# Kernel tuning notes

Hardware: AMD Instinct MI355X
Metric: run time of the kernel (lower is better)

Reference implementation:

```python
import jax, jax.numpy as jnp
import numpy as np

B, S, V, E, H = 256, 512, 800, 128, 256

def setup_inputs() -> dict:
    key = jax.random.key(0)
    ks = jax.random.split(key, 16)
    def rn(k, shape, scale=0.05):
        return jax.random.normal(k, shape, dtype=jnp.float32) * scale
    return {
        "x": jax.random.randint(ks[0], (B, S), 0, V),
        "emb": rn(ks[1], (V, E), 1.0),
        "Wih0": rn(ks[2], (4 * H, E)),
        "Whh0": rn(ks[3], (4 * H, H)),
        "bih0": rn(ks[4], (4 * H,)),
        "bhh0": rn(ks[5], (4 * H,)),
        "Wih1": rn(ks[6], (4 * H, H)),
        "Whh1": rn(ks[7], (4 * H, H)),
        "bih1": rn(ks[8], (4 * H,)),
        "bhh1": rn(ks[9], (4 * H,)),
        "ln_g": jnp.ones((H,), jnp.float32),
        "ln_b": jnp.zeros((H,), jnp.float32),
        "proj_W": rn(ks[10], (E, H)),
        "proj_b": rn(ks[11], (E,)),
    }

def _lstm_layer(x, Wih, Whh, bih, bhh):
    # x: [B, S, D]; returns full hidden sequence [B, S, H]
    b, s, _ = x.shape
    h0 = jnp.zeros((b, H), x.dtype)
    c0 = jnp.zeros((b, H), x.dtype)
    # precompute input projections for all timesteps: [S, B, 4H]
    xp = jnp.einsum("bsd,gd->sbg", x, Wih) + bih + bhh

    def step(carry, xp_t):
        h, c = carry
        gates = xp_t + h @ Whh.T  # [B, 4H]
        i, f, g, o = jnp.split(gates, 4, axis=-1)  # torch gate order i,f,g,o
        i = jax.nn.sigmoid(i)
        f = jax.nn.sigmoid(f)
        g = jnp.tanh(g)
        o = jax.nn.sigmoid(o)
        c = f * c + i * g
        h = o * jnp.tanh(c)
        return (h, c), h

    (_, _), hs = jax.lax.scan(step, (h0, c0), xp)
    return hs.transpose(1, 0, 2)  # [B, S, H]

def reference(x, emb, Wih0, Whh0, bih0, bhh0, Wih1, Whh1, bih1, bhh1, ln_g, ln_b, proj_W, proj_b):
    table = emb.at[0].set(0.0)  # padding_idx=0
    e = table[x]  # [B, S, E]
    h1 = _lstm_layer(e, Wih0, Whh0, bih0, bhh0)
    h2 = _lstm_layer(h1, Wih1, Whh1, bih1, bhh1)
    hn = h2[:, -1, :]  # h_n[-1]: last layer, final timestep [B, H]
    mu = jnp.mean(hn, axis=-1, keepdims=True)
    var = jnp.mean(jnp.square(hn - mu), axis=-1, keepdims=True)
    y = (hn - mu) * jax.lax.rsqrt(var + 1e-5) * ln_g + ln_b
    return y @ proj_W.T + proj_b  # [B, 128]
```

## Files before the change

### kernel.cpp

```cpp
#include <hip/hip_runtime.h>
#include <hip/hip_bf16.h>


typedef unsigned short u16;
typedef unsigned int   u32;
using short8 = __attribute__((ext_vector_type(8))) short;
using f32x4  = __attribute__((ext_vector_type(4))) float;

#define NB 256
#define NS 512
#define NE 128
#define NH 256
#define NG 1024

#define WLDS_FRAGS 18
#define HOFF 147456
#define SCAN_LDS (HOFF + 2 * 16 * NH * 2)

#define L2E     1.4426950408889634f
#define TWO_L2E 2.8853900817779268f

__device__ __forceinline__ u16 f2b(float x) {
  __hip_bfloat16 h = __float2bfloat16(x);
  return __builtin_bit_cast(u16, h);
}
__device__ __forceinline__ float b2f(u16 u) {
  return __builtin_bit_cast(float, (u32)u << 16);
}
__device__ __forceinline__ float ex2(float x)  { return __builtin_amdgcn_exp2f(x); }
__device__ __forceinline__ float ex2n(float x) { return __builtin_amdgcn_exp2f(-x); }
__device__ __forceinline__ float rcpa(float x) { return __builtin_amdgcn_rcpf(x); }

__global__ __launch_bounds__(256) void prep_weights(
    const float* Wih0, const float* Whh0, const float* bih0, const float* bhh0,
    const float* Wih1, const float* Whh1, const float* bih1, const float* bhh1,
    u16* wih0b, u16* whh0b, u16* wih1b, u16* whh1b, float* bc0, float* bc1) {
  int stride = gridDim.x * blockDim.x;
  int tid = blockIdx.x * blockDim.x + threadIdx.x;
  for (int i = tid; i < NG * NE; i += stride) {
    float s = (((i >> 7) >> 8) == 2) ? TWO_L2E : L2E;
    wih0b[i] = f2b(Wih0[i] * s);
  }
  for (int i = tid; i < NG * NH; i += stride) {
    float s = (((i >> 8) >> 8) == 2) ? TWO_L2E : L2E;
    whh0b[i] = f2b(Whh0[i] * s);
    wih1b[i] = f2b(Wih1[i] * s);
    whh1b[i] = f2b(Whh1[i] * s);
  }
  for (int i = tid; i < NG; i += stride) {
    float s = ((i >> 8) == 2) ? TWO_L2E : L2E;
    bc0[i] = (bih0[i] + bhh0[i]) * s;
    bc1[i] = (bih1[i] + bhh1[i]) * s;
  }
}

__global__ __launch_bounds__(256) void embed_chunk(const int* __restrict__ x,
                                                   const float* __restrict__ emb,
                                                   u16* __restrict__ ebuf, int t0) {
  int gid = blockIdx.x * 256 + threadIdx.x;
  int d4 = gid & 31;
  int sb = gid >> 5;
  int b  = sb & (NB - 1);
  int sl = sb >> 8;
  int tok = x[b * NS + (t0 + sl)];
  float4 v = make_float4(0.f, 0.f, 0.f, 0.f);
  if (tok != 0) v = *(const float4*)(emb + (size_t)tok * NE + d4 * 4);
  ushort4 o;
  o.x = f2b(v.x); o.y = f2b(v.y); o.z = f2b(v.z); o.w = f2b(v.w);
  *(ushort4*)(ebuf + (size_t)sb * NE + d4 * 4) = o;
}

template <int K>
__global__ __launch_bounds__(256) void xp_gemm(const u16* __restrict__ A,
                                               const u16* __restrict__ W,
                                               const float* __restrict__ bias,
                                               u16* __restrict__ Cout) {
  __shared__ __align__(16) char lds[2 * 128 * 80];
  char* Asm = lds;
  char* Bsm = lds + 128 * 80;
  int tid = threadIdx.x;
  int w = tid >> 6, l = tid & 63;
  int hi = l >> 4, lo = l & 15;
  int mblk = blockIdx.x >> 3, nblk = blockIdx.x & 7;
  size_t arow0 = (size_t)mblk * 128;
  int g0 = nblk * 128;
  int wm = (w >> 1) * 64, wn = (w & 1) * 64;
  f32x4 acc[4][4] = {};
  int r = tid >> 1, cp = tid & 1;

  for (int k0 = 0; k0 < K; k0 += 32) {
    int4 a0 = *(const int4*)(A + (arow0 + r) * K + k0 + cp * 16);
    int4 a1 = *(const int4*)(A + (arow0 + r) * K + k0 + cp * 16 + 8);
    int4 b0 = *(const int4*)(W + (size_t)(g0 + r) * K + k0 + cp * 16);
    int4 b1 = *(const int4*)(W + (size_t)(g0 + r) * K + k0 + cp * 16 + 8);
    *(int4*)(Asm + r * 80 + cp * 32)      = a0;
    *(int4*)(Asm + r * 80 + cp * 32 + 16) = a1;
    *(int4*)(Bsm + r * 80 + cp * 32)      = b0;
    *(int4*)(Bsm + r * 80 + cp * 32 + 16) = b1;
    __syncthreads();
    short8 af[4], bfr[4];
#pragma unroll
    for (int mt = 0; mt < 4; ++mt)
      af[mt] = *(const short8*)(Asm + (wm + mt * 16 + lo) * 80 + hi * 16);
#pragma unroll
    for (int nt = 0; nt < 4; ++nt)
      bfr[nt] = *(const short8*)(Bsm + (wn + nt * 16 + lo) * 80 + hi * 16);
#pragma unroll
    for (int mt = 0; mt < 4; ++mt)
#pragma unroll
      for (int nt = 0; nt < 4; ++nt)
        acc[mt][nt] = __builtin_amdgcn_mfma_f32_16x16x32_bf16(af[mt], bfr[nt], acc[mt][nt], 0, 0, 0);
    __syncthreads();
  }
#pragma unroll
  for (int nt = 0; nt < 4; ++nt) {
    int gc = g0 + wn + nt * 16 + lo;
    float bv = bias[gc];
    int ws_ = (gc >> 4) & 7, mts = gc >> 7, his = (gc >> 2) & 3, rs = gc & 3;
    size_t gbase = ((size_t)(ws_ * 8 + mts) << 8) + (size_t)(his * 16) * 4 + rs;
#pragma unroll
    for (int mt = 0; mt < 4; ++mt) {
      size_t row = arow0 + wm + mt * 16 + hi * 4;
#pragma unroll
      for (int rr = 0; rr < 4; ++rr) {
        size_t rw = row + rr;
        int t = (int)(rw >> 8), ba = (int)(rw & 255);
        size_t e = ((size_t)(t * 16 + (ba >> 4)) << 14) + gbase + (size_t)(ba & 15) * 4;
        Cout[e] = f2b(acc[mt][nt][rr] + bv);
      }
    }
  }
}

__global__ __launch_bounds__(512, 2)
void scan_stage(const u16* __restrict__ xpA, const u16* __restrict__ whhA,
                u16* __restrict__ houtA, float* __restrict__ hsA,
                float* __restrict__ csA, int firstA, int activeA,
                const u16* __restrict__ xpB, const u16* __restrict__ whhB,
                float* __restrict__ hsB, float* __restrict__ csB,
                int firstB, int activeB,
                const int* __restrict__ x, const float* __restrict__ emb,
                const u16* __restrict__ wih0b, const float* __restrict__ bc0,
                u16* __restrict__ xpC, int t0c, int activeC, int T) {
  extern __shared__ __align__(16) char smem[];
  int bid = blockIdx.x;
  int tid = threadIdx.x;

  if (bid >= 32) {
    if (!activeC) return;
    int team = tid >> 8, tt = tid & 255;
    char* Asm = smem + team * 40960;
    char* Bsm = Asm + 20480;
    int wq = tt >> 6, lq = tt & 63;
    int hiq = lq >> 4, loq = lq & 15;
    int wm = (wq >> 1) * 64, wn = (wq & 1) * 64;
    int r = tt >> 1, cp = tt & 1;
    int njobs = T * 16;
    for (int j = (bid - 32) * 2 + team; j < njobs; j += 64) {
      int mblk = j >> 3, nblk = j & 7;
      size_t arow0 = (size_t)mblk * 128;
      int g0 = nblk * 128;
      f32x4 acc[4][4] = {};
      int rw = (int)(arow0 + r);
      int sl = rw >> 8, ba = rw & 255;
      int tok = x[ba * NS + t0c + sl];
      const float* erow = emb + (size_t)tok * NE;
      for (int k0 = 0; k0 < NE; k0 += 32) {
        const float* src = erow + k0 + cp * 16;
        u32 pk[8];
#pragma unroll
        for (int q = 0; q < 8; ++q) {
          float a = src[2 * q], b = src[2 * q + 1];
          if (tok == 0) { a = 0.0f; b = 0.0f; }
          pk[q] = (u32)f2b(a) | ((u32)f2b(b) << 16);
        }
        *(int4*)(Asm + r * 80 + cp * 32)      = *(int4*)&pk[0];
        *(int4*)(Asm + r * 80 + cp * 32 + 16) = *(int4*)&pk[4];
        int4 b0 = *(const int4*)(wih0b + (size_t)(g0 + r) * NE + k0 + cp * 16);
        int4 b1 = *(const int4*)(wih0b + (size_t)(g0 + r) * NE + k0 + cp * 16 + 8);
        *(int4*)(Bsm + r * 80 + cp * 32)      = b0;
        *(int4*)(Bsm + r * 80 + cp * 32 + 16) = b1;
        __syncthreads();
        short8 af[4], bfr[4];
#pragma unroll
        for (int mt = 0; mt < 4; ++mt)
          af[mt] = *(const short8*)(Asm + (wm + mt * 16 + loq) * 80 + hiq * 16);
#pragma unroll
        for (int nt = 0; nt < 4; ++nt)
          bfr[nt] = *(const short8*)(Bsm + (wn + nt * 16 + loq) * 80 + hiq * 16);
#pragma unroll
        for (int mt = 0; mt < 4; ++mt)
#pragma unroll
          for (int nt = 0; nt < 4; ++nt)
            acc[mt][nt] = __builtin_amdgcn_mfma_f32_16x16x32_bf16(af[mt], bfr[nt], acc[mt][nt], 0, 0, 0);
        __syncthreads();
      }
#pragma unroll
      for (int nt = 0; nt < 4; ++nt) {
        int gc = g0 + wn + nt * 16 + loq;
        float bv = bc0[gc];
        int ws_ = (gc >> 4) & 7, mts = gc >> 7, his = (gc >> 2) & 3, rs = gc & 3;
        size_t gbase = ((size_t)(ws_ * 8 + mts) << 8) + (size_t)(his * 16) * 4 + rs;
#pragma unroll
        for (int mt = 0; mt < 4; ++mt) {
          size_t row = arow0 + wm + mt * 16 + hiq * 4;
#pragma unroll
          for (int rr = 0; rr < 4; ++rr) {
            size_t rw2 = row + rr;
            int t = (int)(rw2 >> 8), ba2 = (int)(rw2 & 255);
            size_t e = ((size_t)(t * 16 + (ba2 >> 4)) << 14) + gbase + (size_t)(ba2 & 15) * 4;
            xpC[e] = f2b(acc[mt][nt][rr] + bv);
          }
        }
      }
    }
    return;
  }

  int roleB = bid >> 4;
  if (roleB ? !activeB : !activeA) return;
  const u16* xp      = roleB ? xpB  : xpA;
  const u16* whh     = roleB ? whhB : whhA;
  u16*       hout    = roleB ? (u16*)0 : houtA;
  float*     h_state = roleB ? hsB : hsA;
  float*     c_state = roleB ? csB : csA;
  int        first   = roleB ? firstB : firstA;
  int bgi = bid & 15;
  int bg = bgi * 16;

  int w = tid >> 6, l = tid & 63;
  int hi = l >> 4, lo = l & 15;

  int wbase = w * (WLDS_FRAGS * 1024) + l * 16;
  short8 wfv[8][5];
  short8 wfv2[6];
#pragma unroll
  for (int mt = 0; mt < 8; ++mt) {
#pragma unroll
    for (int p = 0; p < 8; ++p) {
      const u16* src = whh + (size_t)(16 * (w + 8 * mt) + lo) * NH + p * 32 + hi * 8;
      short8 v = *(const short8*)src;
      if (p < 2)                 *(short8*)(smem + wbase + (p * 8 + mt) * 1024) = v;
      else if (p == 2 && mt < 2) *(short8*)(smem + wbase + (16 + mt) * 1024) = v;
      else if (p == 2)           wfv2[mt - 2] = v;
      else                       wfv[mt][p - 3] = v;
    }
  }

  float c[2][4];
  if (first) {
    for (int i = tid; i < 16 * NH / 2; i += 512) ((u32*)(smem + HOFF))[i] = 0;
#pragma unroll
    for (int g = 0; g < 2; ++g)
#pragma unroll
      for (int r = 0; r < 4; ++r) c[g][r] = 0.0f;
  } else {
    for (int i = tid; i < 16 * NH; i += 512) {
      int b = i >> 8, k = i & 255;
      int p = k >> 5, hp = (k >> 3) & 3, kp = k & 7;
      int xx = hp * 16 + b;
      u16 hb = f2b(h_state[(size_t)(bg + b) * NH + k]);
      *(u16*)(smem + HOFF + p * 1024 + (xx ^ ((xx >> 3) & 7)) * 16 + kp * 2) = hb;
    }
#pragma unroll
    for (int g = 0; g < 2; ++g)
#pragma unroll
      for (int r = 0; r < 4; ++r) {
        int j = 16 * w + 128 * g + hi * 4 + r;
        c[g][r] = c_state[(size_t)(bg + lo) * NH + j];
      }
  }
  __syncthreads();

  int rdoff = (l ^ ((l >> 3) & 7)) * 16;
  int wroff[2];
#pragma unroll
  for (int g = 0; g < 2; ++g) {
    int xx = (2 * (w & 1) + (hi >> 1)) * 16 + lo;
    wroff[g] = (4 * g + (w >> 1)) * 1024 + (xx ^ ((xx >> 3) & 7)) * 16 + 8 * (hi & 1);
  }
  int bq = tid >> 5, kc = tid & 31;
  int xw = (kc & 3) * 16 + bq;
  int wboff = (kc >> 2) * 1024 + (xw ^ ((xw >> 3) & 7)) * 16;
  size_t wb_glob = (size_t)(bg + bq) * NH + kc * 8;

  const u16* xpp = xp + ((size_t)(bgi * 8 + w) * 2048) + (size_t)l * 4;

  ushort4 xq[8];
#pragma unroll
  for (int mt = 0; mt < 8; ++mt) xq[mt] = *(const ushort4*)(xpp + mt * 256);

  f32x4 acc[8];
  for (int t = 0; t < T; ++t) {
    int rbase = HOFF + ((t & 1) << 13);
    int wbbase = HOFF + ((~t & 1) << 13);
#pragma unroll
    for (int mt = 0; mt < 8; ++mt) {
      f32x4 a;
      a[0] = b2f(xq[mt].x); a[1] = b2f(xq[mt].y);
      a[2] = b2f(xq[mt].z); a[3] = b2f(xq[mt].w);
      acc[mt] = a;
    }
    xpp += 262144;
#pragma unroll
    for (int mt = 0; mt < 8; ++mt) xq[mt] = *(const ushort4*)(xpp + mt * 256);
#pragma unroll
    for (int p = 0; p < 8; ++p) {
      short8 bf = *(const short8*)(smem + rbase + rdoff + p * 1024);
#pragma unroll
      for (int mt = 0; mt < 8; ++mt) {
        short8 af;
        if (p < 2)                 af = *(const short8*)(smem + wbase + (p * 8 + mt) * 1024);
        else if (p == 2 && mt < 2) af = *(const short8*)(smem + wbase + (16 + mt) * 1024);
        else if (p == 2)           af = wfv2[mt - 2];
        else                       af = wfv[mt][p - 3];
        acc[mt] = __builtin_amdgcn_mfma_f32_16x16x32_bf16(af, bf, acc[mt], 0, 0, 0);
      }
    }
#pragma unroll
    for (int g = 0; g < 2; ++g) {
      float hv[4];
#pragma unroll
      for (int r = 0; r < 4; ++r) {
        float iv = rcpa(1.0f + ex2n(acc[g][r]));
        float fv = rcpa(1.0f + ex2n(acc[2 + g][r]));
        float gv = 1.0f - 2.0f * rcpa(ex2(acc[4 + g][r]) + 1.0f);
        float ov = rcpa(1.0f + ex2n(acc[6 + g][r]));
        float cc = fv * c[g][r] + iv * gv;
        c[g][r] = cc;
        float th = 1.0f - 2.0f * rcpa(ex2(cc * TWO_L2E) + 1.0f);
        hv[r] = ov * th;
      }
      u32 d0, d1;
      asm("v_cvt_pk_bf16_f32 %0, %1, %2" : "=v"(d0) : "v"(hv[0]), "v"(hv[1]));
      asm("v_cvt_pk_bf16_f32 %0, %1, %2" : "=v"(d1) : "v"(hv[2]), "v"(hv[3]));
      uint2 hw; hw.x = d0; hw.y = d1;
      *(uint2*)(smem + wbbase + wroff[g]) = hw;
    }
    __syncthreads();
    if (hout) {
      int4 hv4 = *(const int4*)(smem + wbbase + wboff);
      *(int4*)(hout + wb_glob + ((size_t)t << 16)) = hv4;
    }
  }

  int fbuf = HOFF + ((T & 1) << 13);
#pragma unroll
  for (int g = 0; g < 2; ++g) {
    ushort4 hv4 = *(const ushort4*)(smem + fbuf + wroff[g]);
    int j = 16 * w + 128 * g + 4 * hi;
    u16 hb[4] = {hv4.x, hv4.y, hv4.z, hv4.w};
#pragma unroll
    for (int r = 0; r < 4; ++r) {
      h_state[(size_t)(bg + lo) * NH + j + r] = b2f(hb[r]);
      c_state[(size_t)(bg + lo) * NH + j + r] = c[g][r];
    }
  }
}

__global__ __launch_bounds__(256) void ln_proj(const float* __restrict__ hn,
                                               const float* __restrict__ lng,
                                               const float* __restrict__ lnb,
                                               const float* __restrict__ pW,
                                               const float* __restrict__ pb,
                                               float* __restrict__ out) {
  __shared__ __align__(16) float nbuf[NH];
  __shared__ float red[8];
  int b = blockIdx.x, tid = threadIdx.x;
  float v = hn[(size_t)b * NH + tid];
  float s = v, s2 = v * v;
#pragma unroll
  for (int o = 32; o > 0; o >>= 1) {
    s  += __shfl_down(s, o);
    s2 += __shfl_down(s2, o);
  }
  if ((tid & 63) == 0) { red[tid >> 6] = s; red[4 + (tid >> 6)] = s2; }
  __syncthreads();
  if (tid == 0) {
    red[0] = red[0] + red[1] + red[2] + red[3];
    red[4] = red[4] + red[5] + red[6] + red[7];
  }
  __syncthreads();
  float mean = red[0] * (1.0f / NH);
  float var  = red[4] * (1.0f / NH) - mean * mean;
  float rs = rsqrtf(var + 1e-5f);
  nbuf[tid] = (v - mean) * rs * lng[tid] + lnb[tid];
  __syncthreads();
  if (tid < NE) {
    float a = pb[tid];
    const float* wr = pW + (size_t)tid * NH;
#pragma unroll 4
    for (int j = 0; j < NH; ++j) a = fmaf(nbuf[j], wr[j], a);
    out[(size_t)b * NE + tid] = a;
  }
}

extern "C" void kernel_launch(void* const* d_in, const int* in_sizes, int n_in,
                              void* d_out, int out_size, void* d_ws, size_t ws_size,
                              hipStream_t stream) {
  const int*   x     = (const int*)d_in[0];
  const float* emb   = (const float*)d_in[1];
  const float* Wih0  = (const float*)d_in[2];
  const float* Whh0  = (const float*)d_in[3];
  const float* bih0  = (const float*)d_in[4];
  const float* bhh0  = (const float*)d_in[5];
  const float* Wih1  = (const float*)d_in[6];
  const float* Whh1  = (const float*)d_in[7];
  const float* bih1  = (const float*)d_in[8];
  const float* bhh1  = (const float*)d_in[9];
  const float* ln_g  = (const float*)d_in[10];
  const float* ln_b  = (const float*)d_in[11];
  const float* projW = (const float*)d_in[12];
  const float* projb = (const float*)d_in[13];

  hipFuncSetAttribute((const void*)scan_stage,
                      hipFuncAttributeMaxDynamicSharedMemorySize, SCAN_LDS);

  const size_t FIXED = 2891776;
  int T = 64;
  while (T > 4 && FIXED + (size_t)T * 1703936 > ws_size) T >>= 1;
  int nch = NS / T;

  char* ws = (char*)d_ws;
  u16*   xpA0  = (u16*)(ws);
  u16*   xpA1  = (u16*)(ws + (size_t)T * 524288);
  u16*   xpB   = (u16*)(ws + (size_t)T * 1048576);
  u16*   iobuf = (u16*)(ws + (size_t)T * 1572864);
  char*  wbase = ws + (size_t)T * 1703936;
  u16*   wih0b = (u16*)(wbase);
  u16*   whh0b = (u16*)(wbase + 262144);
  u16*   wih1b = (u16*)(wbase + 786432);
  u16*   whh1b = (u16*)(wbase + 1310720);
  float* bc0   = (float*)(wbase + 1835008);
  float* bc1   = (float*)(wbase + 1839104);
  float* hs0   = (float*)(wbase + 1843200);
  float* cs0   = (float*)(wbase + 2105344);
  float* hs1   = (float*)(wbase + 2367488);
  float* cs1   = (float*)(wbase + 2629632);
  u16*   xpA[2] = {xpA0, xpA1};

  prep_weights<<<256, 256, 0, stream>>>(Wih0, Whh0, bih0, bhh0, Wih1, Whh1, bih1, bhh1,
                                        wih0b, whh0b, wih1b, whh1b, bc0, bc1);
  embed_chunk<<<T * 32, 256, 0, stream>>>(x, emb, iobuf, 0);
  xp_gemm<NE><<<T * 16, 256, 0, stream>>>(iobuf, wih0b, bc0, xpA0);

  for (int s = 0; s <= nch; ++s) {
    int aA = (s < nch) ? 1 : 0;
    int aB = (s >= 1) ? 1 : 0;
    int aC = (s + 1 < nch) ? 1 : 0;
    scan_stage<<<64, 512, SCAN_LDS, stream>>>(
        xpA[s & 1], whh0b, iobuf, hs0, cs0, (s == 0) ? 1 : 0, aA,
        xpB, whh1b, hs1, cs1, (s == 1) ? 1 : 0, aB,
        x, emb, wih0b, bc0, xpA[(s + 1) & 1], (s + 1) * T, aC, T);
    if (s < nch) {
      xp_gemm<NH><<<T * 16, 256, 0, stream>>>(iobuf, wih1b, bc1, xpB);
    }
  }
  ln_proj<<<NB, 256, 0, stream>>>(hs1, ln_g, ln_b, projW, projb, (float*)d_out);
}
```

Baseline: 1.653 ms.

## Fuse chunked LSTM scan loop into a single persistent kernel with grid barriers

Replaces the per-chunk host loop of scan_stage and xp_gemm launches with one persistent kernel of 224 workgroups. Scan workgroups keep h/c state and weight fragments resident across chunks, so they no longer reload recurrent weights or spill and restore state through global memory between launches. Helper workgroups compute the next chunk's layer-0 input projection and the layer-1 input projection, separated by atomic grid barriers. This removes launch overhead and the serialized xp_gemm launches. It relies on all 224 workgroups being co-resident and adds spin-barrier latency at each phase.

```diff
diff --git a/kernel.cpp b/kernel.cpp
--- a/kernel.cpp
+++ b/kernel.cpp
@@ -17,6 +17,10 @@
 #define HOFF 147456
 #define SCAN_LDS (HOFF + 2 * 16 * NH * 2)
 
+#define NSCAN 32
+#define NHELP 192
+#define NWG   (NSCAN + NHELP)
+
 #define L2E     1.4426950408889634f
 #define TWO_L2E 2.8853900817779268f
 
@@ -30,6 +34,17 @@
 __device__ __forceinline__ float ex2(float x)  { return __builtin_amdgcn_exp2f(x); }
 __device__ __forceinline__ float ex2n(float x) { return __builtin_amdgcn_exp2f(-x); }
 __device__ __forceinline__ float rcpa(float x) { return __builtin_amdgcn_rcpf(x); }
+
+__device__ __forceinline__ void gbar(u32* bar, int ph, int tid) {
+  __syncthreads();
+  if (tid == 0) {
+    __threadfence();
+    __hip_atomic_fetch_add(bar + ph * 16, 1u, __ATOMIC_RELEASE, __HIP_MEMORY_SCOPE_AGENT);
+    while (__hip_atomic_load(bar + ph * 16, __ATOMIC_ACQUIRE, __HIP_MEMORY_SCOPE_AGENT) < (u32)NWG)
+      __builtin_amdgcn_s_sleep(8);
+  }
+  __syncthreads();
+}
 
 __global__ __launch_bounds__(256) void prep_weights(
     const float* Wih0, const float* Whh0, const float* bih0, const float* bhh0,
@@ -52,6 +67,11 @@
     bc0[i] = (bih0[i] + bhh0[i]) * s;
     bc1[i] = (bih1[i] + bhh1[i]) * s;
   }
+}
+
+__global__ __launch_bounds__(256) void zero_flags(u32* f, int n) {
+  int i = blockIdx.x * 256 + threadIdx.x;
+  if (i < n) f[i] = 0;
 }
 
 __global__ __launch_bounds__(256) void embed_chunk(const int* __restrict__ x,
@@ -133,21 +153,19 @@
 }
 
 __global__ __launch_bounds__(512, 2)
-void scan_stage(const u16* __restrict__ xpA, const u16* __restrict__ whhA,
-                u16* __restrict__ houtA, float* __restrict__ hsA,
-                float* __restrict__ csA, int firstA, int activeA,
-                const u16* __restrict__ xpB, const u16* __restrict__ whhB,
-                float* __restrict__ hsB, float* __restrict__ csB,
-                int firstB, int activeB,
-                const int* __restrict__ x, const float* __restrict__ emb,
-                const u16* __restrict__ wih0b, const float* __restrict__ bc0,
-                u16* __restrict__ xpC, int t0c, int activeC, int T) {
+void lstm_persist(const int* __restrict__ x, const float* __restrict__ emb,
+                  const u16* __restrict__ wih0b, const float* __restrict__ bc0,
+                  const u16* __restrict__ whh0b, const u16* __restrict__ whh1b,
+                  const u16* __restrict__ wih1b, const float* __restrict__ bc1,
+                  u16* __restrict__ xpA0, u16* __restrict__ xpA1,
+                  u16* __restrict__ xpB, u16* __restrict__ iobuf,
+                  float* __restrict__ hs1, u32* __restrict__ bar,
+                  int T, int nch) {
   extern __shared__ __align__(16) char smem[];
   int bid = blockIdx.x;
   int tid = threadIdx.x;
 
-  if (bid >= 32) {
-    if (!activeC) return;
+  if (bid >= NSCAN) {
     int team = tid >> 8, tt = tid & 255;
     char* Asm = smem + team * 40960;
     char* Bsm = Asm + 20480;
@@ -155,78 +173,144 @@
     int hiq = lq >> 4, loq = lq & 15;
     int wm = (wq >> 1) * 64, wn = (wq & 1) * 64;
     int r = tt >> 1, cp = tt & 1;
+    int tg = (bid - NSCAN) * 2 + team;
+    const int stride = NHELP * 2;
     int njobs = T * 16;
-    for (int j = (bid - 32) * 2 + team; j < njobs; j += 64) {
-      int mblk = j >> 3, nblk = j & 7;
-      size_t arow0 = (size_t)mblk * 128;
-      int g0 = nblk * 128;
-      f32x4 acc[4][4] = {};
-      int rw = (int)(arow0 + r);
-      int sl = rw >> 8, ba = rw & 255;
-      int tok = x[ba * NS + t0c + sl];
-      const float* erow = emb + (size_t)tok * NE;
-      for (int k0 = 0; k0 < NE; k0 += 32) {
-        const float* src = erow + k0 + cp * 16;
-        u32 pk[8];
-#pragma unroll
-        for (int q = 0; q < 8; ++q) {
-          float a = src[2 * q], b = src[2 * q + 1];
-          if (tok == 0) { a = 0.0f; b = 0.0f; }
-          pk[q] = (u32)f2b(a) | ((u32)f2b(b) << 16);
-        }
-        *(int4*)(Asm + r * 80 + cp * 32)      = *(int4*)&pk[0];
-        *(int4*)(Asm + r * 80 + cp * 32 + 16) = *(int4*)&pk[4];
-        int4 b0 = *(const int4*)(wih0b + (size_t)(g0 + r) * NE + k0 + cp * 16);
-        int4 b1 = *(const int4*)(wih0b + (size_t)(g0 + r) * NE + k0 + cp * 16 + 8);
-        *(int4*)(Bsm + r * 80 + cp * 32)      = b0;
-        *(int4*)(Bsm + r * 80 + cp * 32 + 16) = b1;
-        __syncthreads();
-        short8 af[4], bfr[4];
-#pragma unroll
-        for (int mt = 0; mt < 4; ++mt)
-          af[mt] = *(const short8*)(Asm + (wm + mt * 16 + loq) * 80 + hiq * 16);
-#pragma unroll
-        for (int nt = 0; nt < 4; ++nt)
-          bfr[nt] = *(const short8*)(Bsm + (wn + nt * 16 + loq) * 80 + hiq * 16);
-#pragma unroll
-        for (int mt = 0; mt < 4; ++mt)
-#pragma unroll
-          for (int nt = 0; nt < 4; ++nt)
-            acc[mt][nt] = __builtin_amdgcn_mfma_f32_16x16x32_bf16(af[mt], bfr[nt], acc[mt][nt], 0, 0, 0);
-        __syncthreads();
-      }
-#pragma unroll
-      for (int nt = 0; nt < 4; ++nt) {
-        int gc = g0 + wn + nt * 16 + loq;
-        float bv = bc0[gc];
-        int ws_ = (gc >> 4) & 7, mts = gc >> 7, his = (gc >> 2) & 3, rs = gc & 3;
-        size_t gbase = ((size_t)(ws_ * 8 + mts) << 8) + (size_t)(his * 16) * 4 + rs;
-#pragma unroll
-        for (int mt = 0; mt < 4; ++mt) {
-          size_t row = arow0 + wm + mt * 16 + hiq * 4;
-#pragma unroll
-          for (int rr = 0; rr < 4; ++rr) {
-            size_t rw2 = row + rr;
-            int t = (int)(rw2 >> 8), ba2 = (int)(rw2 & 255);
-            size_t e = ((size_t)(t * 16 + (ba2 >> 4)) << 14) + gbase + (size_t)(ba2 & 15) * 4;
-            xpC[e] = f2b(acc[mt][nt][rr] + bv);
+    int nIt = (njobs + stride - 1) / stride;
+
+    for (int s = 0; s <= nch; ++s) {
+      if (s + 1 < nch) {
+        u16* xpC = ((s + 1) & 1) ? xpA1 : xpA0;
+        int t0c = (s + 1) * T;
+        for (int it = 0; it < nIt; ++it) {
+          int j = tg + it * stride;
+          bool act = j < njobs;
+          int jj = act ? j : 0;
+          int mblk = jj >> 3, nblk = jj & 7;
+          size_t arow0 = (size_t)mblk * 128;
+          int g0 = nblk * 128;
+          f32x4 acc[4][4] = {};
+          int rw = (int)(arow0 + r);
+          int sl = rw >> 8, ba = rw & 255;
+          int tok = x[ba * NS + t0c + sl];
+          const float* erow = emb + (size_t)tok * NE;
+          for (int k0 = 0; k0 < NE; k0 += 32) {
+            const float* src = erow + k0 + cp * 16;
+            u32 pk[8];
+#pragma unroll
+            for (int q = 0; q < 8; ++q) {
+              float a = src[2 * q], b = src[2 * q + 1];
+              if (tok == 0) { a = 0.0f; b = 0.0f; }
+              pk[q] = (u32)f2b(a) | ((u32)f2b(b) << 16);
+            }
+            *(int4*)(Asm + r * 80 + cp * 32)      = *(int4*)&pk[0];
+            *(int4*)(Asm + r * 80 + cp * 32 + 16) = *(int4*)&pk[4];
+            int4 b0 = *(const int4*)(wih0b + (size_t)(g0 + r) * NE + k0 + cp * 16);
+            int4 b1 = *(const int4*)(wih0b + (size_t)(g0 + r) * NE + k0 + cp * 16 + 8);
+            *(int4*)(Bsm + r * 80 + cp * 32)      = b0;
+            *(int4*)(Bsm + r * 80 + cp * 32 + 16) = b1;
+            __syncthreads();
+            short8 af[4], bfr[4];
+#pragma unroll
+            for (int mt = 0; mt < 4; ++mt)
+              af[mt] = *(const short8*)(Asm + (wm + mt * 16 + loq) * 80 + hiq * 16);
+#pragma unroll
+            for (int nt = 0; nt < 4; ++nt)
+              bfr[nt] = *(const short8*)(Bsm + (wn + nt * 16 + loq) * 80 + hiq * 16);
+#pragma unroll
+            for (int mt = 0; mt < 4; ++mt)
+#pragma unroll
+              for (int nt = 0; nt < 4; ++nt)
+                acc[mt][nt] = __builtin_amdgcn_mfma_f32_16x16x32_bf16(af[mt], bfr[nt], acc[mt][nt], 0, 0, 0);
+            __syncthreads();
+          }
+          if (act) {
+#pragma unroll
+            for (int nt = 0; nt < 4; ++nt) {
+              int gc = g0 + wn + nt * 16 + loq;
+              float bv = bc0[gc];
+              int ws_ = (gc >> 4) & 7, mts = gc >> 7, his = (gc >> 2) & 3, rs = gc & 3;
+              size_t gbase = ((size_t)(ws_ * 8 + mts) << 8) + (size_t)(his * 16) * 4 + rs;
+#pragma unroll
+              for (int mt = 0; mt < 4; ++mt) {
+                size_t row = arow0 + wm + mt * 16 + hiq * 4;
+#pragma unroll
+                for (int rr = 0; rr < 4; ++rr) {
+                  size_t rw2 = row + rr;
+                  int t = (int)(rw2 >> 8), ba2 = (int)(rw2 & 255);
+                  size_t e = ((size_t)(t * 16 + (ba2 >> 4)) << 14) + gbase + (size_t)(ba2 & 15) * 4;
+                  xpC[e] = f2b(acc[mt][nt][rr] + bv);
+                }
+              }
+            }
           }
         }
       }
+      gbar(bar, 2 * s, tid);
+      if (s < nch) {
+        for (int it = 0; it < nIt; ++it) {
+          int j = tg + it * stride;
+          bool act = j < njobs;
+          int jj = act ? j : 0;
+          int mblk = jj >> 3, nblk = jj & 7;
+          size_t arow0 = (size_t)mblk * 128;
+          int g0 = nblk * 128;
+          f32x4 acc[4][4] = {};
+          for (int k0 = 0; k0 < NH; k0 += 32) {
+            int4 a0 = *(const int4*)(iobuf + (arow0 + r) * NH + k0 + cp * 16);
+            int4 a1 = *(const int4*)(iobuf + (arow0 + r) * NH + k0 + cp * 16 + 8);
+            int4 b0 = *(const int4*)(wih1b + (size_t)(g0 + r) * NH + k0 + cp * 16);
+            int4 b1 = *(const int4*)(wih1b + (size_t)(g0 + r) * NH + k0 + cp * 16 + 8);
+            *(int4*)(Asm + r * 80 + cp * 32)      = a0;
+            *(int4*)(Asm + r * 80 + cp * 32 + 16) = a1;
+            *(int4*)(Bsm + r * 80 + cp * 32)      = b0;
+            *(int4*)(Bsm + r * 80 + cp * 32 + 16) = b1;
+            __syncthreads();
+            short8 af[4], bfr[4];
+#pragma unroll
+            for (int mt = 0; mt < 4; ++mt)
+              af[mt] = *(const short8*)(Asm + (wm + mt * 16 + loq) * 80 + hiq * 16);
+#pragma unroll
+            for (int nt = 0; nt < 4; ++nt)
+              bfr[nt] = *(const short8*)(Bsm + (wn + nt * 16 + loq) * 80 + hiq * 16);
+#pragma unroll
+            for (int mt = 0; mt < 4; ++mt)
+#pragma unroll
+              for (int nt = 0; nt < 4; ++nt)
+                acc[mt][nt] = __builtin_amdgcn_mfma_f32_16x16x32_bf16(af[mt], bfr[nt], acc[mt][nt], 0, 0, 0);
+            __syncthreads();
+          }
+          if (act) {
+#pragma unroll
+            for (int nt = 0; nt < 4; ++nt) {
+              int gc = g0 + wn + nt * 16 + loq;
+              float bv = bc1[gc];
+              int ws_ = (gc >> 4) & 7, mts = gc >> 7, his = (gc >> 2) & 3, rs = gc & 3;
+              size_t gbase = ((size_t)(ws_ * 8 + mts) << 8) + (size_t)(his * 16) * 4 + rs;
+#pragma unroll
+              for (int mt = 0; mt < 4; ++mt) {
+                size_t row = arow0 + wm + mt * 16 + hiq * 4;
+#pragma unroll
+                for (int rr = 0; rr < 4; ++rr) {
+                  size_t rw2 = row + rr;
+                  int t = (int)(rw2 >> 8), ba2 = (int)(rw2 & 255);
+                  size_t e = ((size_t)(t * 16 + (ba2 >> 4)) << 14) + gbase + (size_t)(ba2 & 15) * 4;
+                  xpB[e] = f2b(acc[mt][nt][rr] + bv);
+                }
+              }
+            }
+          }
+        }
+      }
+      gbar(bar, 2 * s + 1, tid);
     }
     return;
   }
 
   int roleB = bid >> 4;
-  if (roleB ? !activeB : !activeA) return;
-  const u16* xp      = roleB ? xpB  : xpA;
-  const u16* whh     = roleB ? whhB : whhA;
-  u16*       hout    = roleB ? (u16*)0 : houtA;
-  float*     h_state = roleB ? hsB : hsA;
-  float*     c_state = roleB ? csB : csA;
-  int        first   = roleB ? firstB : firstA;
   int bgi = bid & 15;
   int bg = bgi * 16;
+  const u16* whh = roleB ? whh1b : whh0b;
 
   int w = tid >> 6, l = tid & 63;
   int hi = l >> 4, lo = l & 15;
@@ -246,30 +330,12 @@
       else                       wfv[mt][p - 3] = v;
     }
   }
-
   float c[2][4];
-  if (first) {
-    for (int i = tid; i < 16 * NH / 2; i += 512) ((u32*)(smem + HOFF))[i] = 0;
-#pragma unroll
-    for (int g = 0; g < 2; ++g)
-#pragma unroll
-      for (int r = 0; r < 4; ++r) c[g][r] = 0.0f;
-  } else {
-    for (int i = tid; i < 16 * NH; i += 512) {
-      int b = i >> 8, k = i & 255;
-      int p = k >> 5, hp = (k >> 3) & 3, kp = k & 7;
-      int xx = hp * 16 + b;
-      u16 hb = f2b(h_state[(size_t)(bg + b) * NH + k]);
-      *(u16*)(smem + HOFF + p * 1024 + (xx ^ ((xx >> 3) & 7)) * 16 + kp * 2) = hb;
-    }
-#pragma unroll
-    for (int g = 0; g < 2; ++g)
-#pragma unroll
-      for (int r = 0; r < 4; ++r) {
-        int j = 16 * w + 128 * g + hi * 4 + r;
-        c[g][r] = c_state[(size_t)(bg + lo) * NH + j];
-      }
-  }
+  for (int i = tid; i < 16 * NH / 2; i += 512) ((u32*)(smem + HOFF))[i] = 0;
+#pragma unroll
+  for (int g = 0; g < 2; ++g)
+#pragma unroll
+    for (int r = 0; r < 4; ++r) c[g][r] = 0.0f;
   __syncthreads();
 
   int rdoff = (l ^ ((l >> 3) & 7)) * 16;
@@ -284,76 +350,84 @@
   int wboff = (kc >> 2) * 1024 + (xw ^ ((xw >> 3) & 7)) * 16;
   size_t wb_glob = (size_t)(bg + bq) * NH + kc * 8;
 
-  const u16* xpp = xp + ((size_t)(bgi * 8 + w) * 2048) + (size_t)l * 4;
-
-  ushort4 xq[8];
-#pragma unroll
-  for (int mt = 0; mt < 8; ++mt) xq[mt] = *(const ushort4*)(xpp + mt * 256);
-
   f32x4 acc[8];
-  for (int t = 0; t < T; ++t) {
-    int rbase = HOFF + ((t & 1) << 13);
-    int wbbase = HOFF + ((~t & 1) << 13);
-#pragma unroll
-    for (int mt = 0; mt < 8; ++mt) {
-      f32x4 a;
-      a[0] = b2f(xq[mt].x); a[1] = b2f(xq[mt].y);
-      a[2] = b2f(xq[mt].z); a[3] = b2f(xq[mt].w);
-      acc[mt] = a;
-    }
-    xpp += 262144;
-#pragma unroll
-    for (int mt = 0; mt < 8; ++mt) xq[mt] = *(const ushort4*)(xpp + mt * 256);
-#pragma unroll
-    for (int p = 0; p < 8; ++p) {
-      short8 bf = *(const short8*)(smem + rbase + rdoff + p * 1024);
-#pragma unroll
-      for (int mt = 0; mt < 8; ++mt) {
-        short8 af;
-        if (p < 2)                 af = *(const short8*)(smem + wbase + (p * 8 + mt) * 1024);
-        else if (p == 2 && mt < 2) af = *(const short8*)(smem + wbase + (16 + mt) * 1024);
-        else if (p == 2)           af = wfv2[mt - 2];
-        else                       af = wfv[mt][p - 3];
-        acc[mt] = __builtin_amdgcn_mfma_f32_16x16x32_bf16(af, bf, acc[mt], 0, 0, 0);
+  for (int s = 0; s <= nch; ++s) {
+    bool act = roleB ? (s >= 1) : (s < nch);
+    if (act) {
+      int mc = roleB ? (s - 1) : s;
+      const u16* xp = roleB ? xpB : ((mc & 1) ? xpA1 : xpA0);
+      u16* hout = roleB ? (u16*)0 : iobuf;
+      const u16* xpp = xp + ((size_t)(bgi * 8 + w) * 2048) + (size_t)l * 4;
+      ushort4 xq[8];
+#pragma unroll
+      for (int mt = 0; mt < 8; ++mt) xq[mt] = *(const ushort4*)(xpp + mt * 256);
+
+      for (int t = 0; t < T; ++t) {
+        int rbase = HOFF + ((t & 1) << 13);
+        int wbbase = HOFF + ((~t & 1) << 13);
+#pragma unroll
+        for (int mt = 0; mt < 8; ++mt) {
+          f32x4 a;
+          a[0] = b2f(xq[mt].x); a[1] = b2f(xq[mt].y);
+          a[2] = b2f(xq[mt].z); a[3] = b2f(xq[mt].w);
+          acc[mt] = a;
+        }
+        xpp += 262144;
+#pragma unroll
+        for (int mt = 0; mt < 8; ++mt) xq[mt] = *(const ushort4*)(xpp + mt * 256);
+#pragma unroll
+        for (int p = 0; p < 8; ++p) {
+          short8 bf = *(const short8*)(smem + rbase + rdoff + p * 1024);
+#pragma unroll
+          for (int mt = 0; mt < 8; ++mt) {
+            short8 af;
+            if (p < 2)                 af = *(const short8*)(smem + wbase + (p * 8 + mt) * 1024);
+            else if (p == 2 && mt < 2) af = *(const short8*)(smem + wbase + (16 + mt) * 1024);
+            else if (p == 2)           af = wfv2[mt - 2];
+            else                       af = wfv[mt][p - 3];
+            acc[mt] = __builtin_amdgcn_mfma_f32_16x16x32_bf16(af, bf, acc[mt], 0, 0, 0);
+          }
+        }
+#pragma unroll
+        for (int g = 0; g < 2; ++g) {
+          float hv[4];
+#pragma unroll
+          for (int r = 0; r < 4; ++r) {
+            float iv = rcpa(1.0f + ex2n(acc[g][r]));
+            float fv = rcpa(1.0f + ex2n(acc[2 + g][r]));
+            float gv = 1.0f - 2.0f * rcpa(ex2(acc[4 + g][r]) + 1.0f);
+            float ov = rcpa(1.0f + ex2n(acc[6 + g][r]));
+            float cc = fv * c[g][r] + iv * gv;
+            c[g][r] = cc;
+            float th = 1.0f - 2.0f * rcpa(ex2(cc * TWO_L2E) + 1.0f);
+            hv[r] = ov * th;
+          }
+          u32 d0, d1;
+          asm("v_cvt_pk_bf16_f32 %0, %1, %2" : "=v"(d0) : "v"(hv[0]), "v"(hv[1]));
+          asm("v_cvt_pk_bf16_f32 %0, %1, %2" : "=v"(d1) : "v"(hv[2]), "v"(hv[3]));
+          uint2 hw; hw.x = d0; hw.y = d1;
+          *(uint2*)(smem + wbbase + wroff[g]) = hw;
+        }
+        __syncthreads();
+        if (hout) {
+          int4 hv4 = *(const int4*)(smem + wbbase + wboff);
+          *(int4*)(hout + wb_glob + ((size_t)t << 16)) = hv4;
+        }
       }
     }
+    gbar(bar, 2 * s, tid);
+    gbar(bar, 2 * s + 1, tid);
+  }
+
+  if (roleB) {
 #pragma unroll
     for (int g = 0; g < 2; ++g) {
-      float hv[4];
-#pragma unroll
-      for (int r = 0; r < 4; ++r) {
-        float iv = rcpa(1.0f + ex2n(acc[g][r]));
-        float fv = rcpa(1.0f + ex2n(acc[2 + g][r]));
-        float gv = 1.0f - 2.0f * rcpa(ex2(acc[4 + g][r]) + 1.0f);
-        float ov = rcpa(1.0f + ex2n(acc[6 + g][r]));
-        float cc = fv * c[g][r] + iv * gv;
-        c[g][r] = cc;
-        float th = 1.0f - 2.0f * rcpa(ex2(cc * TWO_L2E) + 1.0f);
-        hv[r] = ov * th;
-      }
-      u32 d0, d1;
-      asm("v_cvt_pk_bf16_f32 %0, %1, %2" : "=v"(d0) : "v"(hv[0]), "v"(hv[1]));
-      asm("v_cvt_pk_bf16_f32 %0, %1, %2" : "=v"(d1) : "v"(hv[2]), "v"(hv[3]));
-      uint2 hw; hw.x = d0; hw.y = d1;
-      *(uint2*)(smem + wbbase + wroff[g]) = hw;
-    }
-    __syncthreads();
-    if (hout) {
-      int4 hv4 = *(const int4*)(smem + wbbase + wboff);
-      *(int4*)(hout + wb_glob + ((size_t)t << 16)) = hv4;
-    }
-  }
-
-  int fbuf = HOFF + ((T & 1) << 13);
-#pragma unroll
-  for (int g = 0; g < 2; ++g) {
-    ushort4 hv4 = *(const ushort4*)(smem + fbuf + wroff[g]);
-    int j = 16 * w + 128 * g + 4 * hi;
-    u16 hb[4] = {hv4.x, hv4.y, hv4.z, hv4.w};
-#pragma unroll
-    for (int r = 0; r < 4; ++r) {
-      h_state[(size_t)(bg + lo) * NH + j + r] = b2f(hb[r]);
-      c_state[(size_t)(bg + lo) * NH + j + r] = c[g][r];
+      ushort4 hv4 = *(const ushort4*)(smem + HOFF + wroff[g]);
+      int j = 16 * w + 128 * g + 4 * hi;
+      u16 hb[4] = {hv4.x, hv4.y, hv4.z, hv4.w};
+#pragma unroll
+      for (int r = 0; r < 4; ++r)
+        hs1[(size_t)(bg + lo) * NH + j + r] = b2f(hb[r]);
     }
   }
 }
@@ -413,10 +487,10 @@
   const float* projW = (const float*)d_in[12];
   const float* projb = (const float*)d_in[13];
 
-  hipFuncSetAttribute((const void*)scan_stage,
+  hipFuncSetAttribute((const void*)lstm_persist,
                       hipFuncAttributeMaxDynamicSharedMemorySize, SCAN_LDS);
 
-  const size_t FIXED = 2891776;
+  const size_t FIXED = 2138112;
   int T = 64;
   while (T > 4 && FIXED + (size_t)T * 1703936 > ws_size) T >>= 1;
   int nch = NS / T;
@@ -433,28 +507,18 @@
   u16*   whh1b = (u16*)(wbase + 1310720);
   float* bc0   = (float*)(wbase + 1835008);
   float* bc1   = (float*)(wbase + 1839104);
-  float* hs0   = (float*)(wbase + 1843200);
-  float* cs0   = (float*)(wbase + 2105344);
-  float* hs1   = (float*)(wbase + 2367488);
-  float* cs1   = (float*)(wbase + 2629632);
-  u16*   xpA[2] = {xpA0, xpA1};
-
+  float* hs1   = (float*)(wbase + 1843200);
+  u32*   bar   = (u32*)(wbase + 2105344);
+
+  zero_flags<<<32, 256, 0, stream>>>(bar, 8192);
   prep_weights<<<256, 256, 0, stream>>>(Wih0, Whh0, bih0, bhh0, Wih1, Whh1, bih1, bhh1,
                                         wih0b, whh0b, wih1b, whh1b, bc0, bc1);
   embed_chunk<<<T * 32, 256, 0, stream>>>(x, emb, iobuf, 0);
   xp_gemm<NE><<<T * 16, 256, 0, stream>>>(iobuf, wih0b, bc0, xpA0);
 
-  for (int s = 0; s <= nch; ++s) {
-    int aA = (s < nch) ? 1 : 0;
-    int aB = (s >= 1) ? 1 : 0;
-    int aC = (s + 1 < nch) ? 1 : 0;
-    scan_stage<<<64, 512, SCAN_LDS, stream>>>(
-        xpA[s & 1], whh0b, iobuf, hs0, cs0, (s == 0) ? 1 : 0, aA,
-        xpB, whh1b, hs1, cs1, (s == 1) ? 1 : 0, aB,
-        x, emb, wih0b, bc0, xpA[(s + 1) & 1], (s + 1) * T, aC, T);
-    if (s < nch) {
-      xp_gemm<NH><<<T * 16, 256, 0, stream>>>(iobuf, wih1b, bc1, xpB);
-    }
-  }
+  lstm_persist<<<NWG, 512, SCAN_LDS, stream>>>(
+      x, emb, wih0b, bc0, whh0b, whh1b, wih1b, bc1,
+      xpA0, xpA1, xpB, iobuf, hs1, bar, T, nch);
+
   ln_proj<<<NB, 256, 0, stream>>>(hs1, ln_g, ln_b, projW, projb, (float*)d_out);
 }
```

Result: slower. 4.357 ms, median of 2 (+163.6%).
